# Optimization experiments

Hardware: AMD Instinct MI355X
Metric: run time of the kernel (lower is better)

The kernel has to match this reference:

```python
import jax, jax.numpy as jnp
import numpy as np


def _edge_index(n):
    # all ordered pairs (i, j), i != j -- static since n is a Python int
    ii = np.repeat(np.arange(n), n)
    jj = np.tile(np.arange(n), n)
    m = ii != jj
    return jnp.asarray(ii[m]), jnp.asarray(jj[m])


def _mlp2(x, w1, b1, w2, b2):
    # two Linear layers with ReLU after each (PointNet-style MLP([a,b,c]))
    h = jax.nn.relu(x @ w1 + b1)
    return jax.nn.relu(h @ w2 + b2)


def _fcn(x, w1, b1, w2, b2, w3, b3):
    # FullyConnectedNet: relu(fc1) -> relu(fc2) -> fc3 (no final relu)
    h = jax.nn.relu(x @ w1 + b1)
    h = jax.nn.relu(h @ w2 + b2)
    return h @ w3 + b3


def setup_inputs() -> dict:
    key = jax.random.key(0)
    ks = jax.random.split(key, 32)
    n = 256
    E = n * (n - 1)
    d = 512

    def lin(k, fin, fout):
        k1, k2 = jax.random.split(k)
        s = 1.0 / np.sqrt(fin)
        w = jax.random.uniform(k1, (fin, fout), jnp.float32, -s, s)
        b = jax.random.uniform(k2, (fout,), jnp.float32, -s, s)
        return w, b

    inp = {
        "insnum": n,
        "pred_codes": jax.random.normal(ks[0], (E, d), jnp.float32),
        "bboxes": jax.random.normal(ks[1], (n, 2, 3), jnp.float32),
        "lwhV": jax.random.uniform(ks[2], (n, 3), jnp.float32),
        "centroid": jax.random.normal(ks[3], (n, 3), jnp.float32),
    }
    inp["s_w1"], inp["s_b1"] = lin(ks[4], 512, 512)
    inp["s_w2"], inp["s_b2"] = lin(ks[5], 512, 512)
    inp["p_w1"], inp["p_b1"] = lin(ks[6], 512 + 128, 512)
    inp["p_w2"], inp["p_b2"] = lin(ks[7], 512, 512)
    inp["c_w1"], inp["c_b1"] = lin(ks[8], 512, 512)
    inp["c_w2"], inp["c_b2"] = lin(ks[9], 512, 512)
    inp["l_w1"], inp["l_b1"] = lin(ks[10], 512 * 3, 512)
    inp["l_w2"], inp["l_b2"] = lin(ks[11], 512, 512)
    inp["pos_w1"], inp["pos_b1"] = lin(ks[12], 5, 64)
    inp["pos_w2"], inp["pos_b2"] = lin(ks[13], 64, 64)
    inp["pos_w3"], inp["pos_b3"] = lin(ks[14], 64, 128)
    return inp


def reference(insnum, pred_codes, bboxes, lwhV, centroid,
              s_w1, s_b1, s_w2, s_b2,
              p_w1, p_b1, p_w2, p_b2,
              c_w1, c_b1, c_w2, c_b2,
              l_w1, l_b1, l_w2, l_b2,
              pos_w1, pos_b1, pos_w2, pos_b2, pos_w3, pos_b3):
    src, dst = _edge_index(insnum)
    ci = centroid[src, :2]          # [E, 2]
    cj = centroid[dst, :2]          # [E, 2]
    diff = ci - cj                  # vectorized replacement of per-edge loop
    distance = jnp.linalg.norm(diff, axis=1, keepdims=True)   # [E, 1]
    direction = diff / distance                                # [E, 2]
    pos_features = jnp.concatenate([diff, distance, direction], axis=1)  # [E, 5]

    support_codes = _mlp2(pred_codes, s_w1, s_b1, s_w2, s_b2)
    pos_codes = _fcn(pos_features, pos_w1, pos_b1, pos_w2, pos_b2, pos_w3, pos_b3)
    proximity_features = jnp.concatenate([pred_codes, pos_codes], axis=1)  # [E, 640]
    proximity_codes = _mlp2(proximity_features, p_w1, p_b1, p_w2, p_b2)
    comp_codes = _mlp2(pred_codes, c_w1, c_b1, c_w2, c_b2)
    link_in = jnp.concatenate([support_codes, proximity_codes, comp_codes], axis=1)  # [E, 1536]
    link_codes = _mlp2(link_in, l_w1, l_b1, l_w2, l_b2)
    return (link_codes, support_codes, proximity_codes, comp_codes)
```

## Files before the change

kernel.cpp:

```cpp
#include <hip/hip_runtime.h>
#include <stdint.h>

typedef unsigned short ushort_t;
typedef __attribute__((ext_vector_type(8))) short short8;
typedef __attribute__((ext_vector_type(8))) unsigned short u16x8;
typedef __attribute__((ext_vector_type(4))) float f32x4;

#define GLOBAL_AS __attribute__((address_space(1)))
#define LDS_AS __attribute__((address_space(3)))

__device__ __forceinline__ ushort_t f2bf(float f) {
  union { float f; uint32_t u; } v; v.f = f;
  uint32_t u = v.u;
  u += 0x7FFFu + ((u >> 16) & 1u);
  return (ushort_t)(u >> 16);
}

__device__ __forceinline__ int swz(int row, int byteInRow) {
  return (row * 128 + byteInRow) ^ ((row & 7) << 4);
}

struct TransArgs {
  const float* src[8];
  ushort_t* dst[8];
  int K[8];
  int blk0[9];
};

__global__ __launch_bounds__(256) void transpose_weights(TransArgs ta) {
  __shared__ float tile[64 * 65];
  int b = blockIdx.x;
  int mi = 0;
#pragma unroll
  for (int i = 1; i < 8; ++i) if (b >= ta.blk0[i]) mi = i;
  const float* src = ta.src[mi];
  ushort_t* dst = ta.dst[mi];
  int K = ta.K[mi];
  int rel = b - ta.blk0[mi];
  int ktiles = K >> 6;
  int k0 = (rel % ktiles) << 6;
  int n0 = (rel / ktiles) << 6;
  int t = threadIdx.x;
#pragma unroll
  for (int i = 0; i < 16; ++i) {
    int idx = i * 256 + t;
    int r = idx >> 6, c = idx & 63;
    tile[r * 65 + c] = src[(size_t)(k0 + r) * 512 + (n0 + c)];
  }
  __syncthreads();
#pragma unroll
  for (int i = 0; i < 16; ++i) {
    int idx = i * 256 + t;
    int r = idx >> 6, c = idx & 63;
    dst[(size_t)(n0 + r) * K + (k0 + c)] = f2bf(tile[c * 65 + r]);
  }
}

__global__ __launch_bounds__(256) void prep_kernel(
    const float* __restrict__ pred, const float* __restrict__ centroid,
    const float* __restrict__ pw1, const float* __restrict__ pb1,
    const float* __restrict__ pw2, const float* __restrict__ pb2,
    const float* __restrict__ pw3, const float* __restrict__ pb3,
    ushort_t* __restrict__ X, ushort_t* __restrict__ pos, int nm1)
{
  __shared__ ushort_t h1s[128 * 64];
  __shared__ ushort_t h2s[128 * 64];
  __shared__ ushort_t w2t[64 * 64];
  __shared__ ushort_t w3t[128 * 64];
  __shared__ float w1s[5 * 64];
  __shared__ float b1s[64], b2s[64], b3s[128];
  int t = threadIdx.x;
  for (int idx = t; idx < 64 * 64; idx += 256) {
    int k = idx >> 6, n = idx & 63;
    *(ushort_t*)((char*)w2t + swz(n, k * 2)) = f2bf(pw2[idx]);
  }
  for (int idx = t; idx < 64 * 128; idx += 256) {
    int k = idx >> 7, n = idx & 127;
    *(ushort_t*)((char*)w3t + swz(n, k * 2)) = f2bf(pw3[idx]);
  }
  for (int i = t; i < 5 * 64; i += 256) w1s[i] = pw1[i];
  if (t < 64) { b1s[t] = pb1[t]; b2s[t] = pb2[t]; }
  if (t < 128) b3s[t] = pb3[t];
  __syncthreads();

  int wid = t >> 6, lane = t & 63;
  int ebase = blockIdx.x * 128 + wid * 32;
  for (int it = 0; it < 32; ++it) {
    int e = ebase + it;
    const float* pr = pred + (size_t)e * 512 + lane * 8;
    float4 pA = *(const float4*)pr;
    float4 pB = *(const float4*)(pr + 4);
    u16x8 o;
    o[0] = f2bf(pA.x); o[1] = f2bf(pA.y); o[2] = f2bf(pA.z); o[3] = f2bf(pA.w);
    o[4] = f2bf(pB.x); o[5] = f2bf(pB.y); o[6] = f2bf(pB.z); o[7] = f2bf(pB.w);
    *(u16x8*)(X + (size_t)e * 512 + lane * 8) = o;
    int i = e / nm1;
    int r = e - i * nm1;
    int j = r + (r >= i ? 1 : 0);
    float dx = centroid[i * 3 + 0] - centroid[j * 3 + 0];
    float dy = centroid[i * 3 + 1] - centroid[j * 3 + 1];
    float dist = sqrtf(dx * dx + dy * dy);
    float inv = 1.0f / dist;
    float h1 = w1s[0 * 64 + lane] * dx + w1s[1 * 64 + lane] * dy + w1s[2 * 64 + lane] * dist
             + w1s[3 * 64 + lane] * (dx * inv) + w1s[4 * 64 + lane] * (dy * inv) + b1s[lane];
    h1 = fmaxf(h1, 0.0f);
    int row = wid * 32 + it;
    *(ushort_t*)((char*)h1s + swz(row, lane * 2)) = f2bf(h1);
  }
  __syncthreads();

  int colg = lane & 15, rowg = (lane >> 4) << 2;
  int ko_lane = (lane >> 4) * 8;
  {
    f32x4 acc[2][4];
    f32x4 zero = {0.0f, 0.0f, 0.0f, 0.0f};
#pragma unroll
    for (int m_ = 0; m_ < 2; ++m_)
#pragma unroll
      for (int n_ = 0; n_ < 4; ++n_) acc[m_][n_] = zero;
#pragma unroll
    for (int kk = 0; kk < 2; ++kk) {
      int ko = kk * 32 + ko_lane;
      short8 a[2], b[4];
#pragma unroll
      for (int m_ = 0; m_ < 2; ++m_)
        a[m_] = *(const short8*)((const char*)h1s + swz(wid * 32 + m_ * 16 + colg, ko * 2));
#pragma unroll
      for (int n_ = 0; n_ < 4; ++n_)
        b[n_] = *(const short8*)((const char*)w2t + swz(n_ * 16 + colg, ko * 2));
#pragma unroll
      for (int m_ = 0; m_ < 2; ++m_)
#pragma unroll
        for (int n_ = 0; n_ < 4; ++n_)
          acc[m_][n_] = __builtin_amdgcn_mfma_f32_16x16x32_bf16(a[m_], b[n_], acc[m_][n_], 0, 0, 0);
    }
#pragma unroll
    for (int n_ = 0; n_ < 4; ++n_) {
      int col = n_ * 16 + colg;
      float bv = b2s[col];
#pragma unroll
      for (int m_ = 0; m_ < 2; ++m_) {
        int row = wid * 32 + m_ * 16 + rowg;
#pragma unroll
        for (int jj = 0; jj < 4; ++jj) {
          float v = fmaxf(acc[m_][n_][jj] + bv, 0.0f);
          *(ushort_t*)((char*)h2s + swz(row + jj, col * 2)) = f2bf(v);
        }
      }
    }
  }
  __syncthreads();
  {
    f32x4 acc[2][8];
    f32x4 zero = {0.0f, 0.0f, 0.0f, 0.0f};
#pragma unroll
    for (int m_ = 0; m_ < 2; ++m_)
#pragma unroll
      for (int n_ = 0; n_ < 8; ++n_) acc[m_][n_] = zero;
#pragma unroll
    for (int kk = 0; kk < 2; ++kk) {
      int ko = kk * 32 + ko_lane;
      short8 a[2], b[8];
#pragma unroll
      for (int m_ = 0; m_ < 2; ++m_)
        a[m_] = *(const short8*)((const char*)h2s + swz(wid * 32 + m_ * 16 + colg, ko * 2));
#pragma unroll
      for (int n_ = 0; n_ < 8; ++n_)
        b[n_] = *(const short8*)((const char*)w3t + swz(n_ * 16 + colg, ko * 2));
#pragma unroll
      for (int m_ = 0; m_ < 2; ++m_)
#pragma unroll
        for (int n_ = 0; n_ < 8; ++n_)
          acc[m_][n_] = __builtin_amdgcn_mfma_f32_16x16x32_bf16(a[m_], b[n_], acc[m_][n_], 0, 0, 0);
    }
#pragma unroll
    for (int n_ = 0; n_ < 8; ++n_) {
      int col = n_ * 16 + colg;
      float bv = b3s[col];
#pragma unroll
      for (int m_ = 0; m_ < 2; ++m_) {
        int row = wid * 32 + m_ * 16 + rowg;
#pragma unroll
        for (int jj = 0; jj < 4; ++jj) {
          int e = blockIdx.x * 128 + row + jj;
          pos[(size_t)e * 128 + col] = f2bf(acc[m_][n_][jj] + bv);
        }
      }
    }
  }
}

__global__ __launch_bounds__(256) void gemm_bias_relu(
    const void* __restrict__ A0, int lda0,
    const void* __restrict__ A1, int lda1,
    const void* __restrict__ A2, int lda2,
    int s0, int s1, int aF32,
    const ushort_t* __restrict__ Bt, const float* __restrict__ bias,
    void* __restrict__ Cout, int outF32, ushort_t* __restrict__ Cdual, int K)
{
  __shared__ ushort_t As[128 * 64];
  __shared__ ushort_t Bs[128 * 64];
  int bid = blockIdx.x;
  int cpx = gridDim.x >> 3;
  int swzb = (bid & 7) * cpx + (bid >> 3);
  int mt = swzb >> 2, nt = swzb & 3;
  int m0 = mt << 7, n0 = nt << 7;
  int t = threadIdx.x;
  int lane = t & 63, wid = t >> 6;
  int wm = wid >> 1, wn = wid & 1;
  f32x4 acc[4][4];
  f32x4 zero = {0.0f, 0.0f, 0.0f, 0.0f};
#pragma unroll
  for (int a_ = 0; a_ < 4; ++a_)
#pragma unroll
    for (int b_ = 0; b_ < 4; ++b_) acc[a_][b_] = zero;

  for (int kt = 0; kt < K; kt += 64) {
    const void* Ab; int ldaA; int kin;
    if (kt < s0)      { Ab = A0; ldaA = lda0; kin = kt; }
    else if (kt < s1) { Ab = A1; ldaA = lda1; kin = kt - s0; }
    else              { Ab = A2; ldaA = lda2; kin = kt - s1; }
    if (aF32) {
      const float* Af = (const float*)Ab;
      int rr = t >> 1, cc0 = (t & 1) << 5;
      const float* g = Af + (size_t)(m0 + rr) * ldaA + kin + cc0;
      ushort_t* ldst = As + rr * 64 + cc0;
#pragma unroll
      for (int i = 0; i < 4; ++i) {
        float4 v0 = *(const float4*)(g + i * 8);
        float4 v1 = *(const float4*)(g + i * 8 + 4);
        u16x8 o;
        o[0] = f2bf(v0.x); o[1] = f2bf(v0.y); o[2] = f2bf(v0.z); o[3] = f2bf(v0.w);
        o[4] = f2bf(v1.x); o[5] = f2bf(v1.y); o[6] = f2bf(v1.z); o[7] = f2bf(v1.w);
        *(u16x8*)(ldst + i * 8) = o;
      }
    } else {
      const ushort_t* Ah = (const ushort_t*)Ab;
#pragma unroll
      for (int i = 0; i < 4; ++i) {
        int ch = i * 256 + t;
        int rr = ch >> 3, cc = (ch & 7) << 3;
        const ushort_t* g = Ah + (size_t)(m0 + rr) * ldaA + kin + cc;
        __builtin_amdgcn_global_load_lds((const GLOBAL_AS void*)g,
                                         (LDS_AS void*)(As + ch * 8), 16, 0, 0);
      }
    }
#pragma unroll
    for (int i = 0; i < 4; ++i) {
      int ch = i * 256 + t;
      int rr = ch >> 3, cc = (ch & 7) << 3;
      const ushort_t* g = Bt + (size_t)(n0 + rr) * K + kt + cc;
      __builtin_amdgcn_global_load_lds((const GLOBAL_AS void*)g,
                                       (LDS_AS void*)(Bs + ch * 8), 16, 0, 0);
    }
    __syncthreads();
#pragma unroll
    for (int kk = 0; kk < 64; kk += 32) {
      int ko = kk + (lane >> 4) * 8;
      short8 a[4], b[4];
#pragma unroll
      for (int m_ = 0; m_ < 4; ++m_)
        a[m_] = *(const short8*)(As + (wm * 64 + m_ * 16 + (lane & 15)) * 64 + ko);
#pragma unroll
      for (int n_ = 0; n_ < 4; ++n_)
        b[n_] = *(const short8*)(Bs + (wn * 64 + n_ * 16 + (lane & 15)) * 64 + ko);
#pragma unroll
      for (int m_ = 0; m_ < 4; ++m_)
#pragma unroll
        for (int n_ = 0; n_ < 4; ++n_)
          acc[m_][n_] = __builtin_amdgcn_mfma_f32_16x16x32_bf16(a[m_], b[n_], acc[m_][n_], 0, 0, 0);
    }
    __syncthreads();
  }
  int colg = lane & 15, rowg = (lane >> 4) << 2;
  float* C32 = (float*)Cout;
  ushort_t* C16 = (ushort_t*)Cout;
#pragma unroll
  for (int n_ = 0; n_ < 4; ++n_) {
    int col = n0 + wn * 64 + n_ * 16 + colg;
    float bv = bias[col];
#pragma unroll
    for (int m_ = 0; m_ < 4; ++m_) {
      int row = m0 + wm * 64 + m_ * 16 + rowg;
#pragma unroll
      for (int jj = 0; jj < 4; ++jj) {
        float v = fmaxf(acc[m_][n_][jj] + bv, 0.0f);
        if (outF32) C32[(size_t)(row + jj) * 512 + col] = v;
        else        C16[(size_t)(row + jj) * 512 + col] = f2bf(v);
        if (Cdual)  Cdual[(size_t)(row + jj) * 512 + col] = f2bf(v);
      }
    }
  }
}

extern "C" void kernel_launch(void* const* d_in, const int* in_sizes, int n_in,
                              void* d_out, int out_size, void* d_ws, size_t ws_size,
                              hipStream_t stream) {
  (void)n_in; (void)out_size;
  const float* pred = (const float*)d_in[1];
  const float* centroid = (const float*)d_in[4];
  const float* W[8] = { (const float*)d_in[5],  (const float*)d_in[7],  (const float*)d_in[9],
                        (const float*)d_in[11], (const float*)d_in[13], (const float*)d_in[15],
                        (const float*)d_in[17], (const float*)d_in[19] };
  const float* Bv[8] = { (const float*)d_in[6],  (const float*)d_in[8],  (const float*)d_in[10],
                         (const float*)d_in[12], (const float*)d_in[14], (const float*)d_in[16],
                         (const float*)d_in[18], (const float*)d_in[20] };
  int Kd[8] = {512, 512, 640, 512, 512, 512, 1536, 512};
  const float* pos_w1 = (const float*)d_in[21]; const float* pos_b1 = (const float*)d_in[22];
  const float* pos_w2 = (const float*)d_in[23]; const float* pos_b2 = (const float*)d_in[24];
  const float* pos_w3 = (const float*)d_in[25]; const float* pos_b3 = (const float*)d_in[26];

  int E = in_sizes[1] / 512;
  int n = in_sizes[4] / 3;

  char* ws = (char*)d_ws;
  size_t off = 0;
  auto alloc = [&](size_t bytes) -> void* {
    void* p = ws + off;
    off = (off + bytes + 255) & ~(size_t)255;
    return p;
  };
  size_t SB = (size_t)E * 512 * 2;
  ushort_t* Wt[8];
  for (int i = 0; i < 8; ++i) Wt[i] = (ushort_t*)alloc((size_t)Kd[i] * 512 * 2);
  ushort_t* X = (ushort_t*)alloc(SB);
  size_t base_need = off;
  ushort_t* Hb_ws    = (ushort_t*)alloc(SB);
  ushort_t* sup16_ws = (ushort_t*)alloc(SB);
  bool fast = (off <= ws_size);

  float* outF = (float*)d_out;
  size_t S = (size_t)E * 512;
  float* out_link = outF;
  float* out_sup  = outF + S;
  float* out_prox = outF + 2 * S;
  float* out_comp = outF + 3 * S;
  ushort_t* pos = (ushort_t*)d_out;

  TransArgs ta;
  int nblk = 0;
  for (int i = 0; i < 8; ++i) {
    ta.src[i] = W[i]; ta.dst[i] = Wt[i]; ta.K[i] = Kd[i];
    ta.blk0[i] = nblk;
    nblk += (Kd[i] >> 6) * 8;
  }
  ta.blk0[8] = nblk;
  hipLaunchKernelGGL(transpose_weights, dim3(nblk), dim3(256), 0, stream, ta);
  hipLaunchKernelGGL(prep_kernel, dim3(E / 128), dim3(256), 0, stream,
                     pred, centroid, pos_w1, pos_b1, pos_w2, pos_b2, pos_w3, pos_b3,
                     X, pos, n - 1);

  dim3 g(E / 128 * 4), blk(256);
  const void* Z = nullptr;
  ushort_t* NO16 = nullptr;

  if (fast) {
    ushort_t* prox16 = (ushort_t*)d_out;
    ushort_t* comp16 = X;
    ushort_t* Hl = Hb_ws;
    (void)base_need;
    hipLaunchKernelGGL(gemm_bias_relu, g, blk, 0, stream,
                       (const void*)X, 512, (const void*)pos, 128, Z, 0, 512, 640, 0,
                       Wt[2], Bv[2], (void*)Hb_ws, 0, NO16, 640);
    hipLaunchKernelGGL(gemm_bias_relu, g, blk, 0, stream,
                       (const void*)Hb_ws, 512, Z, 0, Z, 0, 512, 512, 0,
                       Wt[3], Bv[3], (void*)out_prox, 1, prox16, 512);
    hipLaunchKernelGGL(gemm_bias_relu, g, blk, 0, stream,
                       (const void*)X, 512, Z, 0, Z, 0, 512, 512, 0,
                       Wt[0], Bv[0], (void*)Hb_ws, 0, NO16, 512);
    hipLaunchKernelGGL(gemm_bias_relu, g, blk, 0, stream,
                       (const void*)Hb_ws, 512, Z, 0, Z, 0, 512, 512, 0,
                       Wt[1], Bv[1], (void*)out_sup, 1, sup16_ws, 512);
    hipLaunchKernelGGL(gemm_bias_relu, g, blk, 0, stream,
                       (const void*)X, 512, Z, 0, Z, 0, 512, 512, 0,
                       Wt[4], Bv[4], (void*)Hb_ws, 0, NO16, 512);
    hipLaunchKernelGGL(gemm_bias_relu, g, blk, 0, stream,
                       (const void*)Hb_ws, 512, Z, 0, Z, 0, 512, 512, 0,
                       Wt[5], Bv[5], (void*)out_comp, 1, comp16, 512);
    hipLaunchKernelGGL(gemm_bias_relu, g, blk, 0, stream,
                       (const void*)sup16_ws, 512, (const void*)prox16, 512,
                       (const void*)comp16, 512, 512, 1024, 0,
                       Wt[6], Bv[6], (void*)Hl, 0, NO16, 1536);
    hipLaunchKernelGGL(gemm_bias_relu, g, blk, 0, stream,
                       (const void*)Hl, 512, Z, 0, Z, 0, 512, 512, 0,
                       Wt[7], Bv[7], (void*)out_link, 1, NO16, 512);
  } else {
    ushort_t* Hb = (ushort_t*)((char*)d_out + (size_t)32 * 1024 * 1024);
    ushort_t* Hl = X;
    hipLaunchKernelGGL(gemm_bias_relu, g, blk, 0, stream,
                       (const void*)X, 512, (const void*)pos, 128, Z, 0, 512, 640, 0,
                       Wt[2], Bv[2], (void*)Hb, 0, NO16, 640);
    hipLaunchKernelGGL(gemm_bias_relu, g, blk, 0, stream,
                       (const void*)Hb, 512, Z, 0, Z, 0, 512, 512, 0,
                       Wt[3], Bv[3], (void*)out_prox, 1, NO16, 512);
    hipLaunchKernelGGL(gemm_bias_relu, g, blk, 0, stream,
                       (const void*)X, 512, Z, 0, Z, 0, 512, 512, 0,
                       Wt[0], Bv[0], (void*)Hb, 0, NO16, 512);
    hipLaunchKernelGGL(gemm_bias_relu, g, blk, 0, stream,
                       (const void*)Hb, 512, Z, 0, Z, 0, 512, 512, 0,
                       Wt[1], Bv[1], (void*)out_sup, 1, NO16, 512);
    hipLaunchKernelGGL(gemm_bias_relu, g, blk, 0, stream,
                       (const void*)X, 512, Z, 0, Z, 0, 512, 512, 0,
                       Wt[4], Bv[4], (void*)Hb, 0, NO16, 512);
    hipLaunchKernelGGL(gemm_bias_relu, g, blk, 0, stream,
                       (const void*)Hb, 512, Z, 0, Z, 0, 512, 512, 0,
                       Wt[5], Bv[5], (void*)out_comp, 1, NO16, 512);
    hipLaunchKernelGGL(gemm_bias_relu, g, blk, 0, stream,
                       (const void*)out_sup, 512, (const void*)out_prox, 512,
                       (const void*)out_comp, 512, 512, 1024, 1,
                       Wt[6], Bv[6], (void*)Hl, 0, NO16, 1536);
    hipLaunchKernelGGL(gemm_bias_relu, g, blk, 0, stream,
                       (const void*)Hl, 512, Z, 0, Z, 0, 512, 512, 0,
                       Wt[7], Bv[7], (void*)out_link, 1, NO16, 512);
  }
}
```

Before: 807.4 us.

## Add 256x256-tile GEMM with 4-stage direct-to-LDS pipeline and XCD-aware block mapping

Adds a new GEMM kernel with 256x256 output tiles, 512 threads, and a 4-deep ring of direct global-to-LDS loads with swizzled layout. It also remaps block IDs so that consecutive tiles land on the same XCD. The fast path now uses it for all eight layers when E is a multiple of 256. The larger tiles raise operand reuse and cut redundant global reads. The cost is 128KB of LDS, a large accumulator register footprint, and fewer workgroups (E/256*2 = 510), which may leave CUs underused.

```diff
diff --git a/kernel.cpp b/kernel.cpp
--- a/kernel.cpp
+++ b/kernel.cpp
@@ -293,6 +293,121 @@
   }
 }
 
+__global__ __launch_bounds__(512) void gemm256_bias_relu(
+    const ushort_t* __restrict__ A0, int lda0,
+    const ushort_t* __restrict__ A1, int lda1,
+    const ushort_t* __restrict__ A2, int lda2,
+    int s0, int s1,
+    const ushort_t* __restrict__ Bt, const float* __restrict__ bias,
+    void* __restrict__ Cout, int outF32, ushort_t* __restrict__ Cdual, int K)
+{
+  __shared__ ushort_t As[4 * 8192];
+  __shared__ ushort_t Bs[4 * 8192];
+  int bid = blockIdx.x;
+  int nwg = gridDim.x;
+  int q = nwg >> 3, r8 = nwg & 7;
+  int xcd = bid & 7, ii = bid >> 3;
+  int sid = (xcd < r8 ? xcd * (q + 1) : r8 * (q + 1) + (xcd - r8) * q) + ii;
+  int mt = sid >> 1, nt = sid & 1;
+  int m0 = mt << 8, n0 = nt << 8;
+  int t = threadIdx.x;
+  int lane = t & 63, wid = t >> 6;
+  int wm = wid >> 2, wn = wid & 3;
+  int l15 = lane & 15;
+  int kb = (lane >> 4) << 4;
+  int sw = (l15 & 3) << 4;
+  int NT = K >> 5;
+
+  f32x4 acc[8][4];
+  f32x4 zero = {0.0f, 0.0f, 0.0f, 0.0f};
+#pragma unroll
+  for (int mf = 0; mf < 8; ++mf)
+#pragma unroll
+    for (int nf = 0; nf < 4; ++nf) acc[mf][nf] = zero;
+
+  int rA = t >> 2;
+  int cq = (t & 3) << 4;
+
+  auto stage = [&](int tile) {
+    int kt = tile << 5;
+    const ushort_t* Ap; int ld; int kin;
+    if (kt < s0)      { Ap = A0; ld = lda0; kin = kt; }
+    else if (kt < s1) { Ap = A1; ld = lda1; kin = kt - s0; }
+    else              { Ap = A2; ld = lda2; kin = kt - s1; }
+    ushort_t* Ad = As + (size_t)(tile & 3) * 8192;
+    ushort_t* Bd = Bs + (size_t)(tile & 3) * 8192;
+#pragma unroll
+    for (int h = 0; h < 2; ++h) {
+      int row = h * 128 + rA;
+      int cb = cq ^ ((row & 3) << 4);
+      const ushort_t* g = Ap + (size_t)(m0 + row) * ld + kin + (cb >> 1);
+      __builtin_amdgcn_global_load_lds((const GLOBAL_AS void*)g,
+          (LDS_AS void*)(Ad + h * 4096 + t * 8), 16, 0, 0);
+    }
+#pragma unroll
+    for (int h = 0; h < 2; ++h) {
+      int row = h * 128 + rA;
+      int cb = cq ^ ((row & 3) << 4);
+      const ushort_t* g = Bt + (size_t)(n0 + row) * K + kt + (cb >> 1);
+      __builtin_amdgcn_global_load_lds((const GLOBAL_AS void*)g,
+          (LDS_AS void*)(Bd + h * 4096 + t * 8), 16, 0, 0);
+    }
+  };
+
+  stage(0); stage(1); stage(2);
+  asm volatile("s_waitcnt vmcnt(8)" ::: "memory");
+  __builtin_amdgcn_s_barrier();
+  __builtin_amdgcn_sched_barrier(0);
+
+  for (int tt = 0; tt < NT; ++tt) {
+    if (tt + 3 < NT) stage(tt + 3);
+    const char* Ab_ = (const char*)(As + (size_t)(tt & 3) * 8192);
+    const char* Bb_ = (const char*)(Bs + (size_t)(tt & 3) * 8192);
+    short8 b[4];
+#pragma unroll
+    for (int nf = 0; nf < 4; ++nf) {
+      int row = wn * 64 + nf * 16 + l15;
+      b[nf] = *(const short8*)(Bb_ + row * 64 + (kb ^ sw));
+    }
+    __builtin_amdgcn_s_setprio(1);
+#pragma unroll
+    for (int mf = 0; mf < 8; ++mf) {
+      int row = wm * 128 + mf * 16 + l15;
+      short8 a = *(const short8*)(Ab_ + row * 64 + (kb ^ sw));
+#pragma unroll
+      for (int nf = 0; nf < 4; ++nf)
+        acc[mf][nf] = __builtin_amdgcn_mfma_f32_16x16x32_bf16(a, b[nf], acc[mf][nf], 0, 0, 0);
+    }
+    __builtin_amdgcn_s_setprio(0);
+    __builtin_amdgcn_sched_barrier(0);
+    if (tt + 3 < NT)      asm volatile("s_waitcnt vmcnt(8)" ::: "memory");
+    else if (tt + 2 < NT) asm volatile("s_waitcnt vmcnt(4)" ::: "memory");
+    else if (tt + 1 < NT) asm volatile("s_waitcnt vmcnt(0)" ::: "memory");
+    __builtin_amdgcn_s_barrier();
+    __builtin_amdgcn_sched_barrier(0);
+  }
+
+  int colg = l15, rowg = (lane >> 4) << 2;
+  float* C32 = (float*)Cout;
+  ushort_t* C16 = (ushort_t*)Cout;
+#pragma unroll
+  for (int nf = 0; nf < 4; ++nf) {
+    int col = n0 + wn * 64 + nf * 16 + colg;
+    float bv = bias[col];
+#pragma unroll
+    for (int mf = 0; mf < 8; ++mf) {
+      int row = m0 + wm * 128 + mf * 16 + rowg;
+#pragma unroll
+      for (int jj = 0; jj < 4; ++jj) {
+        float v = fmaxf(acc[mf][nf][jj] + bv, 0.0f);
+        if (outF32) C32[(size_t)(row + jj) * 512 + col] = v;
+        else        C16[(size_t)(row + jj) * 512 + col] = f2bf(v);
+        if (Cdual)  Cdual[(size_t)(row + jj) * 512 + col] = f2bf(v);
+      }
+    }
+  }
+}
+
 extern "C" void kernel_launch(void* const* d_in, const int* in_sizes, int n_in,
                               void* d_out, int out_size, void* d_ws, size_t ws_size,
                               hipStream_t stream) {
@@ -324,10 +439,9 @@
   ushort_t* Wt[8];
   for (int i = 0; i < 8; ++i) Wt[i] = (ushort_t*)alloc((size_t)Kd[i] * 512 * 2);
   ushort_t* X = (ushort_t*)alloc(SB);
-  size_t base_need = off;
   ushort_t* Hb_ws    = (ushort_t*)alloc(SB);
   ushort_t* sup16_ws = (ushort_t*)alloc(SB);
-  bool fast = (off <= ws_size);
+  bool fast = (off <= ws_size) && (E % 256 == 0);
 
   float* outF = (float*)d_out;
   size_t S = (size_t)E * 512;
@@ -350,41 +464,42 @@
                      pred, centroid, pos_w1, pos_b1, pos_w2, pos_b2, pos_w3, pos_b3,
                      X, pos, n - 1);
 
-  dim3 g(E / 128 * 4), blk(256);
-  const void* Z = nullptr;
+  const ushort_t* Zu = nullptr;
   ushort_t* NO16 = nullptr;
 
   if (fast) {
+    dim3 g256(E / 256 * 2), b256(512);
     ushort_t* prox16 = (ushort_t*)d_out;
     ushort_t* comp16 = X;
     ushort_t* Hl = Hb_ws;
-    (void)base_need;
-    hipLaunchKernelGGL(gemm_bias_relu, g, blk, 0, stream,
-                       (const void*)X, 512, (const void*)pos, 128, Z, 0, 512, 640, 0,
+    hipLaunchKernelGGL(gemm256_bias_relu, g256, b256, 0, stream,
+                       (const ushort_t*)X, 512, (const ushort_t*)pos, 128, Zu, 0, 512, 640,
                        Wt[2], Bv[2], (void*)Hb_ws, 0, NO16, 640);
-    hipLaunchKernelGGL(gemm_bias_relu, g, blk, 0, stream,
-                       (const void*)Hb_ws, 512, Z, 0, Z, 0, 512, 512, 0,
+    hipLaunchKernelGGL(gemm256_bias_relu, g256, b256, 0, stream,
+                       (const ushort_t*)Hb_ws, 512, Zu, 0, Zu, 0, 512, 512,
                        Wt[3], Bv[3], (void*)out_prox, 1, prox16, 512);
-    hipLaunchKernelGGL(gemm_bias_relu, g, blk, 0, stream,
-                       (const void*)X, 512, Z, 0, Z, 0, 512, 512, 0,
+    hipLaunchKernelGGL(gemm256_bias_relu, g256, b256, 0, stream,
+                       (const ushort_t*)X, 512, Zu, 0, Zu, 0, 512, 512,
                        Wt[0], Bv[0], (void*)Hb_ws, 0, NO16, 512);
-    hipLaunchKernelGGL(gemm_bias_relu, g, blk, 0, stream,
-                       (const void*)Hb_ws, 512, Z, 0, Z, 0, 512, 512, 0,
+    hipLaunchKernelGGL(gemm256_bias_relu, g256, b256, 0, stream,
+                       (const ushort_t*)Hb_ws, 512, Zu, 0, Zu, 0, 512, 512,
                        Wt[1], Bv[1], (void*)out_sup, 1, sup16_ws, 512);
-    hipLaunchKernelGGL(gemm_bias_relu, g, blk, 0, stream,
-                       (const void*)X, 512, Z, 0, Z, 0, 512, 512, 0,
+    hipLaunchKernelGGL(gemm256_bias_relu, g256, b256, 0, stream,
+                       (const ushort_t*)X, 512, Zu, 0, Zu, 0, 512, 512,
                        Wt[4], Bv[4], (void*)Hb_ws, 0, NO16, 512);
-    hipLaunchKernelGGL(gemm_bias_relu, g, blk, 0, stream,
-                       (const void*)Hb_ws, 512, Z, 0, Z, 0, 512, 512, 0,
+    hipLaunchKernelGGL(gemm256_bias_relu, g256, b256, 0, stream,
+                       (const ushort_t*)Hb_ws, 512, Zu, 0, Zu, 0, 512, 512,
                        Wt[5], Bv[5], (void*)out_comp, 1, comp16, 512);
-    hipLaunchKernelGGL(gemm_bias_relu, g, blk, 0, stream,
-                       (const void*)sup16_ws, 512, (const void*)prox16, 512,
-                       (const void*)comp16, 512, 512, 1024, 0,
+    hipLaunchKernelGGL(gemm256_bias_relu, g256, b256, 0, stream,
+                       (const ushort_t*)sup16_ws, 512, (const ushort_t*)prox16, 512,
+                       (const ushort_t*)comp16, 512, 512, 1024,
                        Wt[6], Bv[6], (void*)Hl, 0, NO16, 1536);
-    hipLaunchKernelGGL(gemm_bias_relu, g, blk, 0, stream,
-                       (const void*)Hl, 512, Z, 0, Z, 0, 512, 512, 0,
+    hipLaunchKernelGGL(gemm256_bias_relu, g256, b256, 0, stream,
+                       (const ushort_t*)Hl, 512, Zu, 0, Zu, 0, 512, 512,
                        Wt[7], Bv[7], (void*)out_link, 1, NO16, 512);
   } else {
+    dim3 g(E / 128 * 4), blk(256);
+    const void* Z = nullptr;
     ushort_t* Hb = (ushort_t*)((char*)d_out + (size_t)32 * 1024 * 1024);
     ushort_t* Hl = X;
     hipLaunchKernelGGL(gemm_bias_relu, g, blk, 0, stream,
```

Measured after the change: 885.1 us. 9.6% more time.

## Fuse each two-layer MLP into one kernel keeping hidden activations in LDS

Applied to the files above, without the earlier changes.

Adds a fused_mlp2 kernel that computes both linear+ReLU layers for a 128-row block spanning all 512 output columns. The bf16 hidden tile is kept in 128KB of LDS instead of being written to and reread from global memory. This replaces eight GEMM launches with four and removes the hidden-activation round trips. In exchange, each block reads its B operand straight from global memory with no LDS staging, LDS use is heavy, and there are only E/128 blocks of 512 threads, which may limit occupancy and parallelism.

```diff
diff --git a/kernel.cpp b/kernel.cpp
--- a/kernel.cpp
+++ b/kernel.cpp
@@ -293,6 +293,153 @@
   }
 }
 
+__global__ __launch_bounds__(512, 2) void fused_mlp2(
+    const ushort_t* __restrict__ A0, int lda0,
+    const ushort_t* __restrict__ A1, int lda1,
+    const ushort_t* __restrict__ A2, int lda2,
+    int s0, int s1, int K1,
+    const ushort_t* __restrict__ Wt1, const float* __restrict__ b1,
+    const ushort_t* __restrict__ Wt2, const float* __restrict__ b2,
+    float* __restrict__ outC, ushort_t* __restrict__ dual)
+{
+  __shared__ char lds[131072];
+  int m0 = blockIdx.x * 128;
+  int t = threadIdx.x;
+  int lane = t & 63, wid = t >> 6;
+  int wm = wid >> 2, wn = wid & 3;
+  int g = lane >> 4, l15 = lane & 15;
+
+  f32x4 acc[4][8];
+  f32x4 zero = {0.0f, 0.0f, 0.0f, 0.0f};
+#pragma unroll
+  for (int mf = 0; mf < 4; ++mf)
+#pragma unroll
+    for (int nf = 0; nf < 8; ++nf) acc[mf][nf] = zero;
+
+  auto stageA = [&](int tile) {
+    int kt = tile << 6;
+    const ushort_t* src; int ld; int kin;
+    if (kt < s0)      { src = A0; ld = lda0; kin = kt; }
+    else if (kt < s1) { src = A1; ld = lda1; kin = kt - s0; }
+    else              { src = A2; ld = lda2; kin = kt - s1; }
+    char* dst = lds + (tile & 1) * 16384;
+#pragma unroll
+    for (int L = 0; L < 2; ++L) {
+      int c = wid * 128 + L * 64 + lane;
+      int row = c >> 3;
+      int sl = (c & 7) ^ (row & 7);
+      const ushort_t* gp = src + (size_t)(m0 + row) * ld + kin + sl * 8;
+      __builtin_amdgcn_global_load_lds((const GLOBAL_AS void*)gp,
+          (LDS_AS void*)(dst + c * 16), 16, 0, 0);
+    }
+  };
+
+  float bv[8];
+#pragma unroll
+  for (int nf = 0; nf < 8; ++nf) bv[nf] = b1[wn * 128 + nf * 16 + l15];
+
+  stageA(0);
+  asm volatile("s_waitcnt vmcnt(0)" ::: "memory");
+  __builtin_amdgcn_s_barrier();
+  __builtin_amdgcn_sched_barrier(0);
+
+  int NTa = K1 >> 6;
+  for (int kt = 0; kt < NTa; ++kt) {
+    short8 bf[8][2];
+#pragma unroll
+    for (int nf = 0; nf < 8; ++nf) {
+      int rw = wn * 128 + nf * 16 + l15;
+      const ushort_t* wp = Wt1 + (size_t)rw * K1 + (kt << 6) + g * 8;
+      bf[nf][0] = *(const short8*)(wp);
+      bf[nf][1] = *(const short8*)(wp + 32);
+    }
+    __builtin_amdgcn_sched_barrier(0);
+    asm volatile("s_waitcnt vmcnt(16)" ::: "memory");
+    __builtin_amdgcn_s_barrier();
+    __builtin_amdgcn_sched_barrier(0);
+    if (kt + 1 < NTa) stageA(kt + 1);
+    __builtin_amdgcn_sched_barrier(0);
+    const char* Ab = lds + (kt & 1) * 16384;
+    __builtin_amdgcn_s_setprio(1);
+#pragma unroll
+    for (int mf = 0; mf < 4; ++mf) {
+      int r = wm * 64 + mf * 16 + l15;
+      int sx = (r & 7) << 4;
+      short8 a0 = *(const short8*)(Ab + r * 128 + ((g * 16) ^ sx));
+      short8 a1 = *(const short8*)(Ab + r * 128 + ((64 + g * 16) ^ sx));
+#pragma unroll
+      for (int nf = 0; nf < 8; ++nf) {
+        acc[mf][nf] = __builtin_amdgcn_mfma_f32_16x16x32_bf16(a0, bf[nf][0], acc[mf][nf], 0, 0, 0);
+        acc[mf][nf] = __builtin_amdgcn_mfma_f32_16x16x32_bf16(a1, bf[nf][1], acc[mf][nf], 0, 0, 0);
+      }
+    }
+    __builtin_amdgcn_s_setprio(0);
+    __builtin_amdgcn_sched_barrier(0);
+  }
+
+  __syncthreads();
+#pragma unroll
+  for (int nf = 0; nf < 8; ++nf) {
+    int col = wn * 128 + nf * 16 + l15;
+#pragma unroll
+    for (int mf = 0; mf < 4; ++mf) {
+      int rb = wm * 64 + mf * 16 + (g << 2);
+#pragma unroll
+      for (int jj = 0; jj < 4; ++jj) {
+        int row = rb + jj;
+        float v = fmaxf(acc[mf][nf][jj] + bv[nf], 0.0f);
+        *(ushort_t*)(lds + row * 1024 + ((col * 2) ^ ((row & 7) << 4))) = f2bf(v);
+      }
+    }
+  }
+  __syncthreads();
+
+#pragma unroll
+  for (int mf = 0; mf < 4; ++mf)
+#pragma unroll
+    for (int nf = 0; nf < 8; ++nf) acc[mf][nf] = zero;
+#pragma unroll
+  for (int nf = 0; nf < 8; ++nf) bv[nf] = b2[wn * 128 + nf * 16 + l15];
+
+  for (int kt = 0; kt < 8; ++kt) {
+    short8 a[4][2];
+#pragma unroll
+    for (int mf = 0; mf < 4; ++mf) {
+      int r = wm * 64 + mf * 16 + l15;
+      int sx = (r & 7) << 4;
+      a[mf][0] = *(const short8*)(lds + r * 1024 + ((kt * 128 + g * 16) ^ sx));
+      a[mf][1] = *(const short8*)(lds + r * 1024 + ((kt * 128 + 64 + g * 16) ^ sx));
+    }
+#pragma unroll
+    for (int nf = 0; nf < 8; ++nf) {
+      int rw = wn * 128 + nf * 16 + l15;
+      const ushort_t* wp = Wt2 + (size_t)rw * 512 + (kt << 6) + g * 8;
+      short8 b0 = *(const short8*)(wp);
+      short8 b1f = *(const short8*)(wp + 32);
+#pragma unroll
+      for (int mf = 0; mf < 4; ++mf) {
+        acc[mf][nf] = __builtin_amdgcn_mfma_f32_16x16x32_bf16(a[mf][0], b0, acc[mf][nf], 0, 0, 0);
+        acc[mf][nf] = __builtin_amdgcn_mfma_f32_16x16x32_bf16(a[mf][1], b1f, acc[mf][nf], 0, 0, 0);
+      }
+    }
+  }
+
+#pragma unroll
+  for (int nf = 0; nf < 8; ++nf) {
+    int col = wn * 128 + nf * 16 + l15;
+#pragma unroll
+    for (int mf = 0; mf < 4; ++mf) {
+      int rb = m0 + wm * 64 + mf * 16 + (g << 2);
+#pragma unroll
+      for (int jj = 0; jj < 4; ++jj) {
+        float v = fmaxf(acc[mf][nf][jj] + bv[nf], 0.0f);
+        outC[(size_t)(rb + jj) * 512 + col] = v;
+        if (dual) dual[(size_t)(rb + jj) * 512 + col] = f2bf(v);
+      }
+    }
+  }
+}
+
 extern "C" void kernel_launch(void* const* d_in, const int* in_sizes, int n_in,
                               void* d_out, int out_size, void* d_ws, size_t ws_size,
                               hipStream_t stream) {
@@ -324,10 +471,9 @@
   ushort_t* Wt[8];
   for (int i = 0; i < 8; ++i) Wt[i] = (ushort_t*)alloc((size_t)Kd[i] * 512 * 2);
   ushort_t* X = (ushort_t*)alloc(SB);
-  size_t base_need = off;
-  ushort_t* Hb_ws    = (ushort_t*)alloc(SB);
-  ushort_t* sup16_ws = (ushort_t*)alloc(SB);
-  bool fast = (off <= ws_size);
+  ushort_t* prox16_ws = (ushort_t*)alloc(SB);
+  ushort_t* sup16_ws  = (ushort_t*)alloc(SB);
+  bool fast = (off <= ws_size) && (E % 128 == 0);
 
   float* outF = (float*)d_out;
   size_t S = (size_t)E * 512;
@@ -350,41 +496,28 @@
                      pred, centroid, pos_w1, pos_b1, pos_w2, pos_b2, pos_w3, pos_b3,
                      X, pos, n - 1);
 
-  dim3 g(E / 128 * 4), blk(256);
-  const void* Z = nullptr;
+  const ushort_t* Zu = nullptr;
   ushort_t* NO16 = nullptr;
 
   if (fast) {
-    ushort_t* prox16 = (ushort_t*)d_out;
+    dim3 gf(E / 128), bf(512);
     ushort_t* comp16 = X;
-    ushort_t* Hl = Hb_ws;
-    (void)base_need;
-    hipLaunchKernelGGL(gemm_bias_relu, g, blk, 0, stream,
-                       (const void*)X, 512, (const void*)pos, 128, Z, 0, 512, 640, 0,
-                       Wt[2], Bv[2], (void*)Hb_ws, 0, NO16, 640);
-    hipLaunchKernelGGL(gemm_bias_relu, g, blk, 0, stream,
-                       (const void*)Hb_ws, 512, Z, 0, Z, 0, 512, 512, 0,
-                       Wt[3], Bv[3], (void*)out_prox, 1, prox16, 512);
-    hipLaunchKernelGGL(gemm_bias_relu, g, blk, 0, stream,
-                       (const void*)X, 512, Z, 0, Z, 0, 512, 512, 0,
-                       Wt[0], Bv[0], (void*)Hb_ws, 0, NO16, 512);
-    hipLaunchKernelGGL(gemm_bias_relu, g, blk, 0, stream,
-                       (const void*)Hb_ws, 512, Z, 0, Z, 0, 512, 512, 0,
-                       Wt[1], Bv[1], (void*)out_sup, 1, sup16_ws, 512);
-    hipLaunchKernelGGL(gemm_bias_relu, g, blk, 0, stream,
-                       (const void*)X, 512, Z, 0, Z, 0, 512, 512, 0,
-                       Wt[4], Bv[4], (void*)Hb_ws, 0, NO16, 512);
-    hipLaunchKernelGGL(gemm_bias_relu, g, blk, 0, stream,
-                       (const void*)Hb_ws, 512, Z, 0, Z, 0, 512, 512, 0,
-                       Wt[5], Bv[5], (void*)out_comp, 1, comp16, 512);
-    hipLaunchKernelGGL(gemm_bias_relu, g, blk, 0, stream,
-                       (const void*)sup16_ws, 512, (const void*)prox16, 512,
-                       (const void*)comp16, 512, 512, 1024, 0,
-                       Wt[6], Bv[6], (void*)Hl, 0, NO16, 1536);
-    hipLaunchKernelGGL(gemm_bias_relu, g, blk, 0, stream,
-                       (const void*)Hl, 512, Z, 0, Z, 0, 512, 512, 0,
-                       Wt[7], Bv[7], (void*)out_link, 1, NO16, 512);
+    hipLaunchKernelGGL(fused_mlp2, gf, bf, 0, stream,
+                       (const ushort_t*)X, 512, (const ushort_t*)pos, 128, Zu, 0,
+                       512, 640, 640, Wt[2], Bv[2], Wt[3], Bv[3], out_prox, prox16_ws);
+    hipLaunchKernelGGL(fused_mlp2, gf, bf, 0, stream,
+                       (const ushort_t*)X, 512, Zu, 0, Zu, 0,
+                       512, 512, 512, Wt[0], Bv[0], Wt[1], Bv[1], out_sup, sup16_ws);
+    hipLaunchKernelGGL(fused_mlp2, gf, bf, 0, stream,
+                       (const ushort_t*)X, 512, Zu, 0, Zu, 0,
+                       512, 512, 512, Wt[4], Bv[4], Wt[5], Bv[5], out_comp, comp16);
+    hipLaunchKernelGGL(fused_mlp2, gf, bf, 0, stream,
+                       (const ushort_t*)sup16_ws, 512, (const ushort_t*)prox16_ws, 512,
+                       (const ushort_t*)comp16, 512,
+                       512, 1024, 1536, Wt[6], Bv[6], Wt[7], Bv[7], out_link, NO16);
   } else {
+    dim3 g(E / 128 * 4), blk(256);
+    const void* Z = nullptr;
     ushort_t* Hb = (ushort_t*)((char*)d_out + (size_t)32 * 1024 * 1024);
     ushort_t* Hl = X;
     hipLaunchKernelGGL(gemm_bias_relu, g, blk, 0, stream,
```

Result: slower. 988.4 us (+22.4%).
